# Optimization experiments

Measured on AMD Instinct MI355X. Metric: run time of the kernel, lower is better.

Reference implementation:

```python
import jax, jax.numpy as jnp
import numpy as np

# ---- SS2D hyperparameters (match init_kwargs) ----
B, H, W, D_MODEL = 4, 64, 64, 96
D_STATE = 16
SSM_RATIO = 2
D_INNER = SSM_RATIO * D_MODEL          # 192
DT_RANK = -(-D_MODEL // 16)            # ceil(96/16) = 6
K = 4                                  # 4-way cross scan
D_CONV = 3
LN_EPS = 1e-5


def setup_inputs() -> dict:
    key = jax.random.key(0)
    ks = jax.random.split(key, 8)
    r = lambda i, shape, s: jax.random.normal(ks[i], shape, dtype=jnp.float32) * s
    return {
        "x": jax.random.normal(ks[0], (B, H, W, D_MODEL), dtype=jnp.float32),
        # in_proj: Linear(d_model -> 2*d_inner), bias=False
        "in_proj_w": r(1, (2 * D_INNER, D_MODEL), 0.05),
        # depthwise conv2d: (out=d_inner, in/groups=1, kh, kw), padding 1
        "conv_w": r(2, (D_INNER, 1, D_CONV, D_CONV), 0.1),
        "conv_b": jnp.zeros((D_INNER,), jnp.float32),
        # x_proj_weight: (K, dt_rank + 2*d_state, d_inner)
        "x_proj_weight": r(3, (K, DT_RANK + 2 * D_STATE, D_INNER), 0.05),
        # dt_projs: (K, d_inner, dt_rank) weight, (K, d_inner) bias
        "dt_projs_weight": r(4, (K, D_INNER, DT_RANK), 0.2),
        "dt_projs_bias": r(5, (K, D_INNER), 0.1),
        # A_log = log(arange(1..N)) repeated over K*d_inner channels
        "A_logs": jnp.tile(jnp.log(jnp.arange(1, D_STATE + 1, dtype=jnp.float32))[None, :],
                           (K * D_INNER, 1)),
        "Ds": jnp.ones((K * D_INNER,), jnp.float32),
        "out_norm_w": jnp.ones((D_INNER,), jnp.float32),
        "out_norm_b": jnp.zeros((D_INNER,), jnp.float32),
        # out_proj: Linear(d_inner -> d_model), bias=False
        "out_proj_w": r(6, (D_MODEL, D_INNER), 0.05),
    }


def _cross_scan(x):
    # x: (b, d, h, w) -> xs: (b, 4, d, L)  [row-major, col-major, and their flips]
    b, d, h, w = x.shape
    x0 = x.reshape(b, d, h * w)
    x1 = jnp.swapaxes(x, 2, 3).reshape(b, d, h * w)
    return jnp.stack([x0, x1, x0[..., ::-1], x1[..., ::-1]], axis=1)


def _cross_merge(ys, h, w):
    # ys: (b, 4, d, h, w) -> y: (b, d, L)
    b, k, d = ys.shape[0], ys.shape[1], ys.shape[2]
    ys = ys.reshape(b, k, d, h * w)
    ys = ys[:, 0:2] + ys[:, 2:4][..., ::-1]
    y1 = jnp.swapaxes(ys[:, 1].reshape(b, d, w, h), 2, 3).reshape(b, d, h * w)
    return ys[:, 0] + y1


def _selective_scan(u, dts, A, Bs, Cs, Dskip, delta_bias):
    # u, dts: (b, K, d, L); A: (K, d, N); Bs, Cs: (b, K, N, L)
    # Dskip, delta_bias: (K, d)
    delta = jax.nn.softplus(dts + delta_bias[None, :, :, None])
    u_l = jnp.moveaxis(u, -1, 0)        # (L, b, K, d)
    delta_l = jnp.moveaxis(delta, -1, 0)
    B_l = jnp.moveaxis(Bs, -1, 0)       # (L, b, K, N)
    C_l = jnp.moveaxis(Cs, -1, 0)

    def step(hst, inputs):
        ul, dl, bl, cl = inputs
        dA = jnp.exp(dl[..., None] * A)                       # (b,K,d,N)
        hst = hst * dA + (dl * ul)[..., None] * bl[:, :, None, :]
        y = jnp.einsum('bkdn,bkn->bkd', hst, cl)
        return hst, y

    h0 = jnp.zeros(u_l.shape[1:] + (A.shape[-1],), u.dtype)
    _, ys = jax.lax.scan(step, h0, (u_l, delta_l, B_l, C_l))  # ys: (L,b,K,d)
    ys = jnp.moveaxis(ys, 0, -1)                              # (b,K,d,L)
    return ys + Dskip[None, :, :, None] * u


def reference(x, in_proj_w, conv_w, conv_b, x_proj_weight, dt_projs_weight,
              dt_projs_bias, A_logs, Ds, out_norm_w, out_norm_b, out_proj_w):
    b, h, w, _ = x.shape
    # in_proj then split into ssm branch and gate z
    xz = x @ in_proj_w.T                          # (b,h,w,2*d_inner)
    xin, z = jnp.split(xz, 2, axis=-1)
    # depthwise conv2d (NCHW, OIHW, groups=d_inner) + SiLU
    xc = jnp.transpose(xin, (0, 3, 1, 2))         # (b,d,h,w)
    xc = jax.lax.conv_general_dilated(xc, conv_w, (1, 1), 'SAME',
                                      feature_group_count=D_INNER)
    xc = jax.nn.silu(xc + conv_b[None, :, None, None])

    # cross_selective_scan
    xs = _cross_scan(xc)                                          # (b,4,d,L)
    x_dbl = jnp.einsum('bkdl,kcd->bkcl', xs, x_proj_weight)
    dts, Bs, Cs = jnp.split(x_dbl, [DT_RANK, DT_RANK + D_STATE], axis=2)
    dts = jnp.einsum('bkrl,kdr->bkdl', dts, dt_projs_weight)
    A = -jnp.exp(A_logs).reshape(K, D_INNER, D_STATE)
    ys = _selective_scan(xs, dts, A, Bs, Cs,
                         Ds.reshape(K, D_INNER), dt_projs_bias)   # (b,4,d,L)
    y = _cross_merge(ys.reshape(b, K, D_INNER, h, w), h, w)       # (b,d,L)
    y = jnp.transpose(y, (0, 2, 1)).reshape(b, h, w, D_INNER)

    # out_norm (LayerNorm over d_inner)
    mu = y.mean(-1, keepdims=True)
    var = y.var(-1, keepdims=True)
    y = (y - mu) * jax.lax.rsqrt(var + LN_EPS) * out_norm_w + out_norm_b

    # gate + out_proj
    y = y * jax.nn.silu(z)
    return y @ out_proj_w.T                        # (b,h,w,d_model)
```

## Files before the change

### kernel.cpp

```cpp
#include <hip/hip_runtime.h>
#include <hip/hip_bf16.h>

#define DEV static __device__ __forceinline__

DEV float silu(float x){ return x / (1.f + __expf(-x)); }

typedef __attribute__((ext_vector_type(8))) short bf16x8;
typedef __attribute__((ext_vector_type(4))) float f32x4;

DEV unsigned short f2bf(float f){
    unsigned u = __float_as_uint(f);
    u += 0x7FFF + ((u >> 16) & 1);
    return (unsigned short)(u >> 16);
}
DEV float bf(const unsigned short* p){ return __uint_as_float(((unsigned)(*p)) << 16); }

#define BB 4
#define LL 4096
#define DM 96
#define DI 192
#define NS 16
#define KK 4
#define RR 6
#define C38 38
#define NC 64
#define CL 64
#define NCOMB 224

#define OFF_XIN   0
#define OFF_Z     (OFF_XIN + BB*LL*DI)
#define OFF_XC    (OFF_Z + BB*LL*DI)
#define OFF_DELTA (OFF_XC + BB*LL*DI)
#define OFF_BC    (OFF_DELTA + BB*KK*LL*DI)
#define OFF_YS    (OFF_BC + BB*KK*LL*32)
#define OFF_S     (OFF_YS + BB*KK*LL*DI)
#define OFF_WB    (OFF_S + BB*KK*NC*DI)
#define OFF_CWT   (OFF_WB + 18432)
#define OFF_WC    (OFF_CWT + 1728)
#define OFF_WO    (OFF_WC + 86016)
#define OFF_HLOC  OFF_XIN

DEV int pos_of(int k, int t){
    int pr = ((t & 63) << 6) | (t >> 6);
    int p  = (k & 1) ? pr : t;
    if (k & 2) p = LL - 1 - p;
    return p;
}

__global__ __launch_bounds__(256) void k_prep(const float* __restrict__ win, const float* __restrict__ cw,
                                              const float* __restrict__ xpw, const float* __restrict__ dtw,
                                              const float* __restrict__ wout,
                                              unsigned short* __restrict__ winb, float* __restrict__ cwT,
                                              unsigned short* __restrict__ wcomb, unsigned short* __restrict__ woutb){
    int i = blockIdx.x * 256 + threadIdx.x;
    if (i < 384*DM) winb[i] = f2bf(win[i]);
    if (i < 9*DI){ int tap = i / DI, d = i - tap*DI; cwT[i] = cw[d*9 + tap]; }
    if (i < DM*DI) woutb[i] = f2bf(wout[i]);
    if (i < KK*NCOMB*DI){
        int kk = i % DI; int j = (i / DI) % NCOMB; int k = i / (DI*NCOMB);
        float v;
        if (j < DI){
            v = 0.f;
            const float* dtwp = dtw + ((long)k*DI + j)*RR;
            const float* xp   = xpw + (long)k*C38*DI + kk;
#pragma unroll
            for (int r = 0; r < RR; ++r) v += dtwp[r] * xp[(long)r*DI];
        } else {
            v = xpw[(long)k*C38*DI + (long)(6 + j - DI)*DI + kk];
        }
        wcomb[i] = f2bf(v);
    }
}

__global__ __launch_bounds__(256) void k_inproj(const float* __restrict__ x, const unsigned short* __restrict__ winb,
                                                float* __restrict__ xin, float* __restrict__ z){
    __shared__ unsigned short xsb[16*104];
    int tid = threadIdx.x;
    int r0 = blockIdx.x * 16;
    const float* xrow = x + (long)r0 * DM;
    for (int i = tid; i < 16*DM; i += 256){
        int r = i / DM, d = i - r*DM;
        xsb[r*104 + d] = f2bf(xrow[i]);
    }
    __syncthreads();
    int wv = tid >> 6, l = tid & 63;
    int lrow = l & 15, kg = l >> 4;
    int nc0 = wv * 96;
    f32x4 acc[6];
#pragma unroll
    for (int j = 0; j < 6; ++j) acc[j] = (f32x4){0,0,0,0};
    const unsigned short* arow = &xsb[lrow*104 + kg*8];
#pragma unroll
    for (int kk = 0; kk < 3; ++kk){
        bf16x8 af = *(const bf16x8*)(arow + kk*32);
#pragma unroll
        for (int j = 0; j < 6; ++j){
            int col = nc0 + j*16 + lrow;
            bf16x8 bfr = *(const bf16x8*)(winb + (long)col*DM + kg*8 + kk*32);
            acc[j] = __builtin_amdgcn_mfma_f32_16x16x32_bf16(af, bfr, acc[j], 0,0,0);
        }
    }
#pragma unroll
    for (int j = 0; j < 6; ++j){
        int col = nc0 + j*16 + lrow;
#pragma unroll
        for (int reg = 0; reg < 4; ++reg){
            int row = r0 + kg*4 + reg;
            float v = acc[j][reg];
            if (col < DI) xin[(long)row*DI + col] = v;
            else          z[(long)row*DI + (col - DI)] = v;
        }
    }
}

__global__ __launch_bounds__(256) void k_conv(const float* __restrict__ xin, const float* __restrict__ cwT,
                                              const float* __restrict__ cb, float* __restrict__ xc){
    int g = blockIdx.x * 256 + threadIdx.x;
    int dq = g % 48; int d0 = dq * 4;
    int l = (g / 48) % LL;
    int b = g / (48 * LL);
    int h = l >> 6, wwi = l & 63;
    float4 acc = *(const float4*)(cb + d0);
    const float* base = xin + (long)b * LL * DI + d0;
#pragma unroll
    for (int dy = 0; dy < 3; ++dy){
        int hh = h + dy - 1;
        if (hh < 0 || hh >= 64) continue;
#pragma unroll
        for (int dx = 0; dx < 3; ++dx){
            int wx = wwi + dx - 1;
            if (wx < 0 || wx >= 64) continue;
            float4 xv = *(const float4*)(base + (long)(hh*64 + wx)*DI);
            float4 wv = *(const float4*)(cwT + (dy*3 + dx)*DI + d0);
            acc.x += xv.x*wv.x; acc.y += xv.y*wv.y; acc.z += xv.z*wv.z; acc.w += xv.w*wv.w;
        }
    }
    float4 o;
    o.x = silu(acc.x); o.y = silu(acc.y); o.z = silu(acc.z); o.w = silu(acc.w);
    *(float4*)(xc + ((long)b*LL + l)*DI + d0) = o;
}

#define XP 200
__global__ __launch_bounds__(256) void k_xdbl(const float* __restrict__ xc, const unsigned short* __restrict__ wcomb,
                                              const float* __restrict__ dtb,
                                              unsigned short* __restrict__ delta, float* __restrict__ bc2){
    __shared__ unsigned short xsb[64*XP];
    int tid = threadIdx.x;
    int bk   = blockIdx.x >> 6;
    int tile = blockIdx.x & 63;
    int b = bk >> 2, k = bk & 3;
    int t0 = tile * 64;
    for (int i = tid; i < 64*48; i += 256){
        int r = i / 48, q = i - r*48;
        int p = pos_of(k, t0 + r);
        float4 v = *(const float4*)(xc + ((long)b*LL + p)*DI + q*4);
        ushort4 o;
        o.x = f2bf(v.x); o.y = f2bf(v.y); o.z = f2bf(v.z); o.w = f2bf(v.w);
        *(ushort4*)(&xsb[r*XP + q*4]) = o;
    }
    __syncthreads();

    int wv = tid >> 6, l = tid & 63;
    int lrow = l & 15, kgrp = l >> 4;
    int ch = wv & 1, rh = wv >> 1;
    f32x4 acc[2][7];
#pragma unroll
    for (int rt = 0; rt < 2; ++rt)
#pragma unroll
        for (int j = 0; j < 7; ++j) acc[rt][j] = (f32x4){0,0,0,0};
    const unsigned short* arow0 = &xsb[(rh*32 + lrow)*XP + kgrp*8];
    const unsigned short* arow1 = &xsb[(rh*32 + 16 + lrow)*XP + kgrp*8];
    const unsigned short* wb = wcomb + (long)k*NCOMB*DI + ((long)ch*112 + lrow)*DI + kgrp*8;
#pragma unroll
    for (int ks = 0; ks < 6; ++ks){
        bf16x8 bfr[7];
#pragma unroll
        for (int nt = 0; nt < 7; ++nt)
            bfr[nt] = *(const bf16x8*)(wb + (long)nt*16*DI + ks*32);
        bf16x8 a0 = *(const bf16x8*)(arow0 + ks*32);
        bf16x8 a1 = *(const bf16x8*)(arow1 + ks*32);
#pragma unroll
        for (int nt = 0; nt < 7; ++nt)
            acc[0][nt] = __builtin_amdgcn_mfma_f32_16x16x32_bf16(a0, bfr[nt], acc[0][nt], 0,0,0);
#pragma unroll
        for (int nt = 0; nt < 7; ++nt)
            acc[1][nt] = __builtin_amdgcn_mfma_f32_16x16x32_bf16(a1, bfr[nt], acc[1][nt], 0,0,0);
    }
#pragma unroll
    for (int rt = 0; rt < 2; ++rt){
        long obase = (long)bk*LL + t0 + rh*32 + rt*16 + kgrp*4;
#pragma unroll
        for (int nt = 0; nt < 7; ++nt){
            int col = ch*112 + nt*16 + lrow;
            if (col < DI){
                float bias = dtb[k*DI + col];
#pragma unroll
                for (int reg = 0; reg < 4; ++reg){
                    float raw = acc[rt][nt][reg] + bias;
                    float sp = (raw > 15.f) ? raw : __logf(1.f + __expf(raw));
                    delta[(obase + reg)*DI + col] = f2bf(sp);
                }
            } else {
                int q = col - DI;
#pragma unroll
                for (int reg = 0; reg < 4; ++reg)
                    bc2[(obase + reg)*32 + q] = acc[rt][nt][reg];
            }
        }
    }
}

__global__ __launch_bounds__(192) void k_scanA(const unsigned short* __restrict__ delta, const float* __restrict__ bc2,
                                               const float* __restrict__ xc, const float* __restrict__ alog,
                                               float* __restrict__ hloc, float* __restrict__ Ssum){
    int d = threadIdx.x;
    int bid = blockIdx.x;
    int c = bid & 63; int bk = bid >> 6;
    int b = bk >> 2, k = bk & 3;
    float a[NS]; bool fast = true;
#pragma unroll
    for (int n = 0; n < NS; ++n){
        a[n] = -__expf(alog[(k*DI + d)*NS + n]);
        fast = fast && (fabsf(a[n] + (float)(n + 1)) < 1e-4f*(float)(n + 1));
    }
    int t0 = c * CL;
    int p0, st;
    if (k == 0){ p0 = t0;         st = 1;   }
    else if (k == 1){ p0 = c;     st = 64;  }
    else if (k == 2){ p0 = LL-1-t0; st = -1;  }
    else            { p0 = LL-1-c;  st = -64; }
    const unsigned short* dep = delta + ((long)bk*LL + t0)*DI + d;
    const float* bcp = bc2   + ((long)bk*LL + t0)*32;
    const float* up  = xc + ((long)b*LL + p0)*DI + d;
    long ustep = (long)st * DI;
    float h[NS];
#pragma unroll
    for (int n = 0; n < NS; ++n) h[n] = 0.f;
    float S = 0.f;
    if (fast){
        float de = bf(dep), u = *up;
        const float4* bq = (const float4*)bcp;
        float4 b0 = bq[0], b1 = bq[1], b2 = bq[2], b3 = bq[3];
        for (int i = 0; i < CL; ++i){
            dep += DI; up += ustep; bcp += 32;
            float de_n = bf(dep);
            float u_n  = *up;
            const float4* bqn = (const float4*)bcp;
            float4 b0n = bqn[0], b1n = bqn[1], b2n = bqn[2], b3n = bqn[3];
            float P[NS];
            P[0] = __expf(-de);
            P[1] = P[0]*P[0];
#pragma unroll
            for (int n = 2; n < NS; ++n) P[n] = P[(n-1)>>1] * P[n-1-((n-1)>>1)];
            float du = de * u;
            S += de;
            float bb[NS] = {b0.x,b0.y,b0.z,b0.w, b1.x,b1.y,b1.z,b1.w,
                            b2.x,b2.y,b2.z,b2.w, b3.x,b3.y,b3.z,b3.w};
#pragma unroll
            for (int n = 0; n < NS; ++n) h[n] = h[n]*P[n] + du*bb[n];
            de = de_n; u = u_n; b0 = b0n; b1 = b1n; b2 = b2n; b3 = b3n;
        }
    } else {
        for (int i = 0; i < CL; ++i){
            float de = bf(dep);
            float u  = *up;
            const float4* bq = (const float4*)bcp;
            float4 b0 = bq[0], b1 = bq[1], b2 = bq[2], b3 = bq[3];
            float du = de * u;
            S += de;
            float bb[NS] = {b0.x,b0.y,b0.z,b0.w, b1.x,b1.y,b1.z,b1.w,
                            b2.x,b2.y,b2.z,b2.w, b3.x,b3.y,b3.z,b3.w};
#pragma unroll
            for (int n = 0; n < NS; ++n){ float dA = __expf(de*a[n]); h[n] = h[n]*dA + du*bb[n]; }
            dep += DI; up += ustep; bcp += 32;
        }
    }
    long ho = (((long)bk*NC + c)*DI + d)*NS;
#pragma unroll
    for (int q = 0; q < 4; ++q)
        *(float4*)(hloc + ho + q*4) = make_float4(h[q*4],h[q*4+1],h[q*4+2],h[q*4+3]);
    Ssum[((long)bk*NC + c)*DI + d] = S;
}

__global__ __launch_bounds__(256) void k_scanB(float* __restrict__ hloc, const float* __restrict__ Ssum,
                                               const float* __restrict__ alog){
    int gid = blockIdx.x * 256 + threadIdx.x;
    int dn = gid % (DI*NS);
    int bk = gid / (DI*NS);
    int d = dn >> 4, n = dn & 15;
    int k = bk & 3;
    float a = -__expf(alog[(k*DI + d)*NS + n]);
    float h = 0.f;
    long o     = (long)bk * NC * DI * NS + dn;
    long sbase = (long)bk * NC * DI + d;
    float Sc  = Ssum[sbase];
    float tmp = hloc[o];
    for (int c = 0; c < NC; ++c){
        long o_n = o + (long)DI*NS;
        float Sc_n  = Ssum[sbase + (long)(c+1)*DI];
        float tmp_n = hloc[o_n];
        float P = __expf(a * Sc);
        hloc[o] = h;
        h = h * P + tmp;
        o = o_n; Sc = Sc_n; tmp = tmp_n;
    }
}

__global__ __launch_bounds__(192) void k_scanC(const unsigned short* __restrict__ delta, const float* __restrict__ bc2,
                                               const float* __restrict__ xc, const float* __restrict__ alog,
                                               const float* __restrict__ hloc, unsigned short* __restrict__ ys){
    int d = threadIdx.x;
    int bid = blockIdx.x;
    int c = bid & 63; int bk = bid >> 6;
    int b = bk >> 2, k = bk & 3;
    float a[NS]; bool fast = true;
#pragma unroll
    for (int n = 0; n < NS; ++n){
        a[n] = -__expf(alog[(k*DI + d)*NS + n]);
        fast = fast && (fabsf(a[n] + (float)(n + 1)) < 1e-4f*(float)(n + 1));
    }
    int t0 = c * CL;
    int p0, st;
    if (k == 0){ p0 = t0;         st = 1;   }
    else if (k == 1){ p0 = c;     st = 64;  }
    else if (k == 2){ p0 = LL-1-t0; st = -1;  }
    else            { p0 = LL-1-c;  st = -64; }
    const unsigned short* dep = delta + ((long)bk*LL + t0)*DI + d;
    const float* bcp = bc2   + ((long)bk*LL + t0)*32;
    const float* up  = xc + ((long)b*LL + p0)*DI + d;
    unsigned short* yp = ys + ((long)bk*LL + p0)*DI + d;
    long ustep = (long)st * DI;
    long ho = (((long)bk*NC + c)*DI + d)*NS;
    float h[NS];
#pragma unroll
    for (int q = 0; q < 4; ++q){
        float4 hv = *(const float4*)(hloc + ho + q*4);
        h[q*4] = hv.x; h[q*4+1] = hv.y; h[q*4+2] = hv.z; h[q*4+3] = hv.w;
    }
    if (fast){
        float de = bf(dep), u = *up;
        const float4* bq = (const float4*)bcp;
        float4 b0 = bq[0], b1 = bq[1], b2 = bq[2], b3 = bq[3];
        float4 c0 = bq[4], c1 = bq[5], c2 = bq[6], c3 = bq[7];
        for (int i = 0; i < CL; ++i){
            dep += DI; up += ustep; bcp += 32;
            float de_n = bf(dep);
            float u_n  = *up;
            const float4* bqn = (const float4*)bcp;
            float4 b0n = bqn[0], b1n = bqn[1], b2n = bqn[2], b3n = bqn[3];
            float4 c0n = bqn[4], c1n = bqn[5], c2n = bqn[6], c3n = bqn[7];
            float P[NS];
            P[0] = __expf(-de);
            P[1] = P[0]*P[0];
#pragma unroll
            for (int n = 2; n < NS; ++n) P[n] = P[(n-1)>>1] * P[n-1-((n-1)>>1)];
            float du = de * u;
            float bb[NS] = {b0.x,b0.y,b0.z,b0.w, b1.x,b1.y,b1.z,b1.w,
                            b2.x,b2.y,b2.z,b2.w, b3.x,b3.y,b3.z,b3.w};
            float cc[NS] = {c0.x,c0.y,c0.z,c0.w, c1.x,c1.y,c1.z,c1.w,
                            c2.x,c2.y,c2.z,c2.w, c3.x,c3.y,c3.z,c3.w};
            float y = 0.f;
#pragma unroll
            for (int n = 0; n < NS; ++n){ h[n] = h[n]*P[n] + du*bb[n]; y += h[n]*cc[n]; }
            *yp = f2bf(y);
            yp += ustep;
            de = de_n; u = u_n;
            b0 = b0n; b1 = b1n; b2 = b2n; b3 = b3n;
            c0 = c0n; c1 = c1n; c2 = c2n; c3 = c3n;
        }
    } else {
        for (int i = 0; i < CL; ++i){
            float de = bf(dep);
            float u  = *up;
            const float4* bq = (const float4*)bcp;
            float4 b0 = bq[0], b1 = bq[1], b2 = bq[2], b3 = bq[3];
            float4 c0 = bq[4], c1 = bq[5], c2 = bq[6], c3 = bq[7];
            float du = de * u;
            float bb[NS] = {b0.x,b0.y,b0.z,b0.w, b1.x,b1.y,b1.z,b1.w,
                            b2.x,b2.y,b2.z,b2.w, b3.x,b3.y,b3.z,b3.w};
            float cc[NS] = {c0.x,c0.y,c0.z,c0.w, c1.x,c1.y,c1.z,c1.w,
                            c2.x,c2.y,c2.z,c2.w, c3.x,c3.y,c3.z,c3.w};
            float y = 0.f;
#pragma unroll
            for (int n = 0; n < NS; ++n){ float dA = __expf(de*a[n]); h[n] = h[n]*dA + du*bb[n]; y += h[n]*cc[n]; }
            *yp = f2bf(y);
            dep += DI; up += ustep; yp += ustep; bcp += 32;
        }
    }
}

__global__ __launch_bounds__(256) void k_fuse(const unsigned short* __restrict__ ys, const float* __restrict__ xc,
                                              const float* __restrict__ z, const float* __restrict__ Dsk,
                                              const float* __restrict__ lnw, const float* __restrict__ lnb,
                                              const unsigned short* __restrict__ woutb, float* __restrict__ out){
    __shared__ unsigned short gt[32*200];
    int tid = threadIdx.x;
    int wv = tid >> 6, l = tid & 63;
    int b  = blockIdx.x / (LL/32);
    int p0 = (blockIdx.x % (LL/32)) * 32;
    float sumD[3], lw[3], lb[3];
#pragma unroll
    for (int q = 0; q < 3; ++q){
        int d = l + q*64;
        sumD[q] = Dsk[d] + Dsk[DI + d] + Dsk[2*DI + d] + Dsk[3*DI + d];
        lw[q] = lnw[d]; lb[q] = lnb[d];
    }
    for (int pass = 0; pass < 8; ++pass){
        int pl = wv*8 + pass;
        int p = p0 + pl;
        long base = (long)b*LL + p;
        float yv[3], zv[3];
        float s = 0.f, sq = 0.f;
#pragma unroll
        for (int q = 0; q < 3; ++q){
            int d = l + q*64;
            long yo = ((long)(b*4)*LL + p)*DI + d;
            float y = bf(ys + yo) + bf(ys + yo + (long)LL*DI)
                    + bf(ys + yo + 2L*LL*DI) + bf(ys + yo + 3L*LL*DI);
            y += xc[base*DI + d] * sumD[q];
            zv[q] = z[base*DI + d];
            yv[q] = y; s += y; sq += y*y;
        }
#pragma unroll
        for (int m = 32; m > 0; m >>= 1){ s += __shfl_xor(s, m, 64); sq += __shfl_xor(sq, m, 64); }
        float mu = s / DI, var = sq / DI - mu*mu;
        float rs = rsqrtf(var + 1e-5f);
#pragma unroll
        for (int q = 0; q < 3; ++q){
            int d = l + q*64;
            float yn = (yv[q] - mu)*rs*lw[q] + lb[q];
            gt[pl*200 + d] = f2bf(yn * silu(zv[q]));
        }
    }
    __syncthreads();
    int lrow = l & 15, kg = l >> 4;
    int rt = wv & 1, cp = wv >> 1;
    f32x4 acc[3];
#pragma unroll
    for (int j = 0; j < 3; ++j) acc[j] = (f32x4){0,0,0,0};
    const unsigned short* arow = &gt[(rt*16 + lrow)*200 + kg*8];
    const unsigned short* wbase = woutb + ((long)cp*48 + lrow)*DI + kg*8;
#pragma unroll
    for (int ks = 0; ks < 6; ++ks){
        bf16x8 af = *(const bf16x8*)(arow + ks*32);
#pragma unroll
        for (int nt = 0; nt < 3; ++nt){
            bf16x8 bfr = *(const bf16x8*)(wbase + (long)nt*16*DI + ks*32);
            acc[nt] = __builtin_amdgcn_mfma_f32_16x16x32_bf16(af, bfr, acc[nt], 0,0,0);
        }
    }
#pragma unroll
    for (int nt = 0; nt < 3; ++nt){
        int m = cp*48 + nt*16 + lrow;
#pragma unroll
        for (int reg = 0; reg < 4; ++reg){
            int pl = rt*16 + kg*4 + reg;
            out[((long)b*LL + p0 + pl)*DM + m] = acc[nt][reg];
        }
    }
}

extern "C" void kernel_launch(void* const* d_in, const int* in_sizes, int n_in,
                              void* d_out, int out_size, void* d_ws, size_t ws_size,
                              hipStream_t stream){
    (void)in_sizes; (void)n_in; (void)out_size; (void)ws_size;
    const float* x    = (const float*)d_in[0];
    const float* win  = (const float*)d_in[1];
    const float* cw   = (const float*)d_in[2];
    const float* cb   = (const float*)d_in[3];
    const float* xpw  = (const float*)d_in[4];
    const float* dtw  = (const float*)d_in[5];
    const float* dtb  = (const float*)d_in[6];
    const float* alog = (const float*)d_in[7];
    const float* ds   = (const float*)d_in[8];
    const float* lnw  = (const float*)d_in[9];
    const float* lnb  = (const float*)d_in[10];
    const float* wout = (const float*)d_in[11];

    float* ws    = (float*)d_ws;
    float* xin   = ws + OFF_XIN;
    float* z     = ws + OFF_Z;
    float* xc    = ws + OFF_XC;
    unsigned short* delta = (unsigned short*)(ws + OFF_DELTA);
    float* bc2   = ws + OFF_BC;
    unsigned short* ysb = (unsigned short*)(ws + OFF_YS);
    float* Ssum  = ws + OFF_S;
    unsigned short* winb  = (unsigned short*)(ws + OFF_WB);
    float* cwT   = ws + OFF_CWT;
    unsigned short* wcomb = (unsigned short*)(ws + OFF_WC);
    unsigned short* woutb = (unsigned short*)(ws + OFF_WO);
    float* hloc  = ws + OFF_HLOC;

    k_prep  <<<dim3(672),  dim3(256), 0, stream>>>(win, cw, xpw, dtw, wout, winb, cwT, wcomb, woutb);
    k_inproj<<<dim3(1024), dim3(256), 0, stream>>>(x, winb, xin, z);
    k_conv  <<<dim3(3072), dim3(256), 0, stream>>>(xin, cwT, cb, xc);
    k_xdbl  <<<dim3(1024), dim3(256), 0, stream>>>(xc, wcomb, dtb, delta, bc2);
    k_scanA <<<dim3(1024), dim3(192), 0, stream>>>(delta, bc2, xc, alog, hloc, Ssum);
    k_scanB <<<dim3(192),  dim3(256), 0, stream>>>(hloc, Ssum, alog);
    k_scanC <<<dim3(1024), dim3(192), 0, stream>>>(delta, bc2, xc, alog, hloc, ysb);
    k_fuse  <<<dim3(512),  dim3(256), 0, stream>>>(ysb, xc, z, ds, lnw, lnb, woutb,
                                                   (float*)d_out);
}
```

Baseline: 163.0 us.

## Fuse x_proj/dt_proj GEMM into both scan passes, recomputing through LDS

Removes the standalone k_xdbl kernel and the global delta/B/C buffers. Each scan pass (A and C) now recomputes the per-chunk MFMA projection into shared memory and runs the chunk recurrence from LDS. This cuts the large global write and re-read of delta and B/C. In exchange the GEMM runs twice, each block holds about 56KB of LDS, which limits occupancy, and only 192 of 256 threads run the scan. The scan input u is also now read as bf16 instead of fp32.

```diff
diff --git a/kernel.cpp b/kernel.cpp
--- a/kernel.cpp
+++ b/kernel.cpp
@@ -30,9 +30,7 @@
 #define OFF_XIN   0
 #define OFF_Z     (OFF_XIN + BB*LL*DI)
 #define OFF_XC    (OFF_Z + BB*LL*DI)
-#define OFF_DELTA (OFF_XC + BB*LL*DI)
-#define OFF_BC    (OFF_DELTA + BB*KK*LL*DI)
-#define OFF_YS    (OFF_BC + BB*KK*LL*32)
+#define OFF_YS    (OFF_XC + BB*LL*DI)
 #define OFF_S     (OFF_YS + BB*KK*LL*DI)
 #define OFF_WB    (OFF_S + BB*KK*NC*DI)
 #define OFF_CWT   (OFF_WB + 18432)
@@ -141,15 +139,74 @@
 }
 
 #define XP 200
-__global__ __launch_bounds__(256) void k_xdbl(const float* __restrict__ xc, const unsigned short* __restrict__ wcomb,
-                                              const float* __restrict__ dtb,
-                                              unsigned short* __restrict__ delta, float* __restrict__ bc2){
+
+template<int BS, bool WANT_C>
+DEV void gemm_phase(int tid, int k, const unsigned short* __restrict__ wcomb,
+                    const float* __restrict__ dtb,
+                    const unsigned short* xsb, unsigned short* dlds, float* blds){
+    int wv = tid >> 6, l = tid & 63;
+    int lrow = l & 15, kgrp = l >> 4;
+    int ch = wv & 1, rh = wv >> 1;
+    f32x4 acc[2][7];
+#pragma unroll
+    for (int rt = 0; rt < 2; ++rt)
+#pragma unroll
+        for (int j = 0; j < 7; ++j) acc[rt][j] = (f32x4){0,0,0,0};
+    const unsigned short* arow0 = &xsb[(rh*32 + lrow)*XP + kgrp*8];
+    const unsigned short* arow1 = &xsb[(rh*32 + 16 + lrow)*XP + kgrp*8];
+    const unsigned short* wb = wcomb + (long)k*NCOMB*DI + ((long)ch*112 + lrow)*DI + kgrp*8;
+#pragma unroll
+    for (int ks = 0; ks < 6; ++ks){
+        bf16x8 bfr[7];
+#pragma unroll
+        for (int nt = 0; nt < 7; ++nt)
+            bfr[nt] = *(const bf16x8*)(wb + (long)nt*16*DI + ks*32);
+        bf16x8 a0 = *(const bf16x8*)(arow0 + ks*32);
+        bf16x8 a1 = *(const bf16x8*)(arow1 + ks*32);
+#pragma unroll
+        for (int nt = 0; nt < 7; ++nt)
+            acc[0][nt] = __builtin_amdgcn_mfma_f32_16x16x32_bf16(a0, bfr[nt], acc[0][nt], 0,0,0);
+#pragma unroll
+        for (int nt = 0; nt < 7; ++nt)
+            acc[1][nt] = __builtin_amdgcn_mfma_f32_16x16x32_bf16(a1, bfr[nt], acc[1][nt], 0,0,0);
+    }
+#pragma unroll
+    for (int rt = 0; rt < 2; ++rt){
+        int rowb = rh*32 + rt*16 + kgrp*4;
+#pragma unroll
+        for (int nt = 0; nt < 7; ++nt){
+            int col = ch*112 + nt*16 + lrow;
+            if (col < DI){
+                float bias = dtb[k*DI + col];
+#pragma unroll
+                for (int reg = 0; reg < 4; ++reg){
+                    float raw = acc[rt][nt][reg] + bias;
+                    float sp = (raw > 15.f) ? raw : __logf(1.f + __expf(raw));
+                    dlds[(rowb + reg)*XP + col] = f2bf(sp);
+                }
+            } else {
+                int q = col - DI;
+                if (WANT_C || q < 16){
+#pragma unroll
+                    for (int reg = 0; reg < 4; ++reg)
+                        blds[(rowb + reg)*BS + q] = acc[rt][nt][reg];
+                }
+            }
+        }
+    }
+}
+
+#define BSA 20
+__global__ __launch_bounds__(256) void k_scanAf(const float* __restrict__ xc, const unsigned short* __restrict__ wcomb,
+                                                const float* __restrict__ dtb, const float* __restrict__ alog,
+                                                float* __restrict__ hloc, float* __restrict__ Ssum){
     __shared__ unsigned short xsb[64*XP];
+    __shared__ unsigned short dlds[64*XP];
+    __shared__ float blds[64*BSA];
     int tid = threadIdx.x;
-    int bk   = blockIdx.x >> 6;
-    int tile = blockIdx.x & 63;
+    int c = blockIdx.x & 63; int bk = blockIdx.x >> 6;
     int b = bk >> 2, k = bk & 3;
-    int t0 = tile * 64;
+    int t0 = c * CL;
     for (int i = tid; i < 64*48; i += 256){
         int r = i / 48, q = i - r*48;
         int p = pos_of(k, t0 + r);
@@ -159,127 +216,58 @@
         *(ushort4*)(&xsb[r*XP + q*4]) = o;
     }
     __syncthreads();
-
-    int wv = tid >> 6, l = tid & 63;
-    int lrow = l & 15, kgrp = l >> 4;
-    int ch = wv & 1, rh = wv >> 1;
-    f32x4 acc[2][7];
-#pragma unroll
-    for (int rt = 0; rt < 2; ++rt)
-#pragma unroll
-        for (int j = 0; j < 7; ++j) acc[rt][j] = (f32x4){0,0,0,0};
-    const unsigned short* arow0 = &xsb[(rh*32 + lrow)*XP + kgrp*8];
-    const unsigned short* arow1 = &xsb[(rh*32 + 16 + lrow)*XP + kgrp*8];
-    const unsigned short* wb = wcomb + (long)k*NCOMB*DI + ((long)ch*112 + lrow)*DI + kgrp*8;
-#pragma unroll
-    for (int ks = 0; ks < 6; ++ks){
-        bf16x8 bfr[7];
-#pragma unroll
-        for (int nt = 0; nt < 7; ++nt)
-            bfr[nt] = *(const bf16x8*)(wb + (long)nt*16*DI + ks*32);
-        bf16x8 a0 = *(const bf16x8*)(arow0 + ks*32);
-        bf16x8 a1 = *(const bf16x8*)(arow1 + ks*32);
-#pragma unroll
-        for (int nt = 0; nt < 7; ++nt)
-            acc[0][nt] = __builtin_amdgcn_mfma_f32_16x16x32_bf16(a0, bfr[nt], acc[0][nt], 0,0,0);
-#pragma unroll
-        for (int nt = 0; nt < 7; ++nt)
-            acc[1][nt] = __builtin_amdgcn_mfma_f32_16x16x32_bf16(a1, bfr[nt], acc[1][nt], 0,0,0);
-    }
-#pragma unroll
-    for (int rt = 0; rt < 2; ++rt){
-        long obase = (long)bk*LL + t0 + rh*32 + rt*16 + kgrp*4;
-#pragma unroll
-        for (int nt = 0; nt < 7; ++nt){
-            int col = ch*112 + nt*16 + lrow;
-            if (col < DI){
-                float bias = dtb[k*DI + col];
-#pragma unroll
-                for (int reg = 0; reg < 4; ++reg){
-                    float raw = acc[rt][nt][reg] + bias;
-                    float sp = (raw > 15.f) ? raw : __logf(1.f + __expf(raw));
-                    delta[(obase + reg)*DI + col] = f2bf(sp);
-                }
-            } else {
-                int q = col - DI;
-#pragma unroll
-                for (int reg = 0; reg < 4; ++reg)
-                    bc2[(obase + reg)*32 + q] = acc[rt][nt][reg];
+    gemm_phase<BSA, false>(tid, k, wcomb, dtb, xsb, dlds, blds);
+    __syncthreads();
+    if (tid < DI){
+        int d = tid;
+        float a[NS]; bool fast = true;
+#pragma unroll
+        for (int n = 0; n < NS; ++n){
+            a[n] = -__expf(alog[(k*DI + d)*NS + n]);
+            fast = fast && (fabsf(a[n] + (float)(n + 1)) < 1e-4f*(float)(n + 1));
+        }
+        float h[NS];
+#pragma unroll
+        for (int n = 0; n < NS; ++n) h[n] = 0.f;
+        float S = 0.f;
+        if (fast){
+            for (int i = 0; i < CL; ++i){
+                float de = bf(&dlds[i*XP + d]);
+                float u  = bf(&xsb[i*XP + d]);
+                const float4* bq = (const float4*)&blds[i*BSA];
+                float4 b0 = bq[0], b1 = bq[1], b2 = bq[2], b3 = bq[3];
+                float P[NS];
+                P[0] = __expf(-de);
+                P[1] = P[0]*P[0];
+#pragma unroll
+                for (int n = 2; n < NS; ++n) P[n] = P[(n-1)>>1] * P[n-1-((n-1)>>1)];
+                float du = de * u;
+                S += de;
+                float bb[NS] = {b0.x,b0.y,b0.z,b0.w, b1.x,b1.y,b1.z,b1.w,
+                                b2.x,b2.y,b2.z,b2.w, b3.x,b3.y,b3.z,b3.w};
+#pragma unroll
+                for (int n = 0; n < NS; ++n) h[n] = h[n]*P[n] + du*bb[n];
             }
-        }
-    }
-}
-
-__global__ __launch_bounds__(192) void k_scanA(const unsigned short* __restrict__ delta, const float* __restrict__ bc2,
-                                               const float* __restrict__ xc, const float* __restrict__ alog,
-                                               float* __restrict__ hloc, float* __restrict__ Ssum){
-    int d = threadIdx.x;
-    int bid = blockIdx.x;
-    int c = bid & 63; int bk = bid >> 6;
-    int b = bk >> 2, k = bk & 3;
-    float a[NS]; bool fast = true;
-#pragma unroll
-    for (int n = 0; n < NS; ++n){
-        a[n] = -__expf(alog[(k*DI + d)*NS + n]);
-        fast = fast && (fabsf(a[n] + (float)(n + 1)) < 1e-4f*(float)(n + 1));
-    }
-    int t0 = c * CL;
-    int p0, st;
-    if (k == 0){ p0 = t0;         st = 1;   }
-    else if (k == 1){ p0 = c;     st = 64;  }
-    else if (k == 2){ p0 = LL-1-t0; st = -1;  }
-    else            { p0 = LL-1-c;  st = -64; }
-    const unsigned short* dep = delta + ((long)bk*LL + t0)*DI + d;
-    const float* bcp = bc2   + ((long)bk*LL + t0)*32;
-    const float* up  = xc + ((long)b*LL + p0)*DI + d;
-    long ustep = (long)st * DI;
-    float h[NS];
-#pragma unroll
-    for (int n = 0; n < NS; ++n) h[n] = 0.f;
-    float S = 0.f;
-    if (fast){
-        float de = bf(dep), u = *up;
-        const float4* bq = (const float4*)bcp;
-        float4 b0 = bq[0], b1 = bq[1], b2 = bq[2], b3 = bq[3];
-        for (int i = 0; i < CL; ++i){
-            dep += DI; up += ustep; bcp += 32;
-            float de_n = bf(dep);
-            float u_n  = *up;
-            const float4* bqn = (const float4*)bcp;
-            float4 b0n = bqn[0], b1n = bqn[1], b2n = bqn[2], b3n = bqn[3];
-            float P[NS];
-            P[0] = __expf(-de);
-            P[1] = P[0]*P[0];
-#pragma unroll
-            for (int n = 2; n < NS; ++n) P[n] = P[(n-1)>>1] * P[n-1-((n-1)>>1)];
-            float du = de * u;
-            S += de;
-            float bb[NS] = {b0.x,b0.y,b0.z,b0.w, b1.x,b1.y,b1.z,b1.w,
-                            b2.x,b2.y,b2.z,b2.w, b3.x,b3.y,b3.z,b3.w};
-#pragma unroll
-            for (int n = 0; n < NS; ++n) h[n] = h[n]*P[n] + du*bb[n];
-            de = de_n; u = u_n; b0 = b0n; b1 = b1n; b2 = b2n; b3 = b3n;
-        }
-    } else {
-        for (int i = 0; i < CL; ++i){
-            float de = bf(dep);
-            float u  = *up;
-            const float4* bq = (const float4*)bcp;
-            float4 b0 = bq[0], b1 = bq[1], b2 = bq[2], b3 = bq[3];
-            float du = de * u;
-            S += de;
-            float bb[NS] = {b0.x,b0.y,b0.z,b0.w, b1.x,b1.y,b1.z,b1.w,
-                            b2.x,b2.y,b2.z,b2.w, b3.x,b3.y,b3.z,b3.w};
-#pragma unroll
-            for (int n = 0; n < NS; ++n){ float dA = __expf(de*a[n]); h[n] = h[n]*dA + du*bb[n]; }
-            dep += DI; up += ustep; bcp += 32;
-        }
-    }
-    long ho = (((long)bk*NC + c)*DI + d)*NS;
-#pragma unroll
-    for (int q = 0; q < 4; ++q)
-        *(float4*)(hloc + ho + q*4) = make_float4(h[q*4],h[q*4+1],h[q*4+2],h[q*4+3]);
-    Ssum[((long)bk*NC + c)*DI + d] = S;
+        } else {
+            for (int i = 0; i < CL; ++i){
+                float de = bf(&dlds[i*XP + d]);
+                float u  = bf(&xsb[i*XP + d]);
+                const float4* bq = (const float4*)&blds[i*BSA];
+                float4 b0 = bq[0], b1 = bq[1], b2 = bq[2], b3 = bq[3];
+                float du = de * u;
+                S += de;
+                float bb[NS] = {b0.x,b0.y,b0.z,b0.w, b1.x,b1.y,b1.z,b1.w,
+                                b2.x,b2.y,b2.z,b2.w, b3.x,b3.y,b3.z,b3.w};
+#pragma unroll
+                for (int n = 0; n < NS; ++n){ float dA = __expf(de*a[n]); h[n] = h[n]*dA + du*bb[n]; }
+            }
+        }
+        long ho = (((long)bk*NC + c)*DI + d)*NS;
+#pragma unroll
+        for (int q = 0; q < 4; ++q)
+            *(float4*)(hloc + ho + q*4) = make_float4(h[q*4],h[q*4+1],h[q*4+2],h[q*4+3]);
+        Ssum[((long)bk*NC + c)*DI + d] = S;
+    }
 }
 
 __global__ __launch_bounds__(256) void k_scanB(float* __restrict__ hloc, const float* __restrict__ Ssum,
@@ -306,85 +294,91 @@
     }
 }
 
-__global__ __launch_bounds__(192) void k_scanC(const unsigned short* __restrict__ delta, const float* __restrict__ bc2,
-                                               const float* __restrict__ xc, const float* __restrict__ alog,
-                                               const float* __restrict__ hloc, unsigned short* __restrict__ ys){
-    int d = threadIdx.x;
-    int bid = blockIdx.x;
-    int c = bid & 63; int bk = bid >> 6;
+#define BSC 36
+__global__ __launch_bounds__(256) void k_scanCf(const float* __restrict__ xc, const unsigned short* __restrict__ wcomb,
+                                                const float* __restrict__ dtb, const float* __restrict__ alog,
+                                                const float* __restrict__ hloc, unsigned short* __restrict__ ys){
+    __shared__ unsigned short xsb[64*XP];
+    __shared__ unsigned short dlds[64*XP];
+    __shared__ float blds[64*BSC];
+    int tid = threadIdx.x;
+    int c = blockIdx.x & 63; int bk = blockIdx.x >> 6;
     int b = bk >> 2, k = bk & 3;
-    float a[NS]; bool fast = true;
-#pragma unroll
-    for (int n = 0; n < NS; ++n){
-        a[n] = -__expf(alog[(k*DI + d)*NS + n]);
-        fast = fast && (fabsf(a[n] + (float)(n + 1)) < 1e-4f*(float)(n + 1));
-    }
     int t0 = c * CL;
-    int p0, st;
-    if (k == 0){ p0 = t0;         st = 1;   }
-    else if (k == 1){ p0 = c;     st = 64;  }
-    else if (k == 2){ p0 = LL-1-t0; st = -1;  }
-    else            { p0 = LL-1-c;  st = -64; }
-    const unsigned short* dep = delta + ((long)bk*LL + t0)*DI + d;
-    const float* bcp = bc2   + ((long)bk*LL + t0)*32;
-    const float* up  = xc + ((long)b*LL + p0)*DI + d;
-    unsigned short* yp = ys + ((long)bk*LL + p0)*DI + d;
-    long ustep = (long)st * DI;
-    long ho = (((long)bk*NC + c)*DI + d)*NS;
-    float h[NS];
-#pragma unroll
-    for (int q = 0; q < 4; ++q){
-        float4 hv = *(const float4*)(hloc + ho + q*4);
-        h[q*4] = hv.x; h[q*4+1] = hv.y; h[q*4+2] = hv.z; h[q*4+3] = hv.w;
-    }
-    if (fast){
-        float de = bf(dep), u = *up;
-        const float4* bq = (const float4*)bcp;
-        float4 b0 = bq[0], b1 = bq[1], b2 = bq[2], b3 = bq[3];
-        float4 c0 = bq[4], c1 = bq[5], c2 = bq[6], c3 = bq[7];
-        for (int i = 0; i < CL; ++i){
-            dep += DI; up += ustep; bcp += 32;
-            float de_n = bf(dep);
-            float u_n  = *up;
-            const float4* bqn = (const float4*)bcp;
-            float4 b0n = bqn[0], b1n = bqn[1], b2n = bqn[2], b3n = bqn[3];
-            float4 c0n = bqn[4], c1n = bqn[5], c2n = bqn[6], c3n = bqn[7];
-            float P[NS];
-            P[0] = __expf(-de);
-            P[1] = P[0]*P[0];
-#pragma unroll
-            for (int n = 2; n < NS; ++n) P[n] = P[(n-1)>>1] * P[n-1-((n-1)>>1)];
-            float du = de * u;
-            float bb[NS] = {b0.x,b0.y,b0.z,b0.w, b1.x,b1.y,b1.z,b1.w,
-                            b2.x,b2.y,b2.z,b2.w, b3.x,b3.y,b3.z,b3.w};
-            float cc[NS] = {c0.x,c0.y,c0.z,c0.w, c1.x,c1.y,c1.z,c1.w,
-                            c2.x,c2.y,c2.z,c2.w, c3.x,c3.y,c3.z,c3.w};
-            float y = 0.f;
-#pragma unroll
-            for (int n = 0; n < NS; ++n){ h[n] = h[n]*P[n] + du*bb[n]; y += h[n]*cc[n]; }
-            *yp = f2bf(y);
-            yp += ustep;
-            de = de_n; u = u_n;
-            b0 = b0n; b1 = b1n; b2 = b2n; b3 = b3n;
-            c0 = c0n; c1 = c1n; c2 = c2n; c3 = c3n;
-        }
-    } else {
-        for (int i = 0; i < CL; ++i){
-            float de = bf(dep);
-            float u  = *up;
-            const float4* bq = (const float4*)bcp;
-            float4 b0 = bq[0], b1 = bq[1], b2 = bq[2], b3 = bq[3];
-            float4 c0 = bq[4], c1 = bq[5], c2 = bq[6], c3 = bq[7];
-            float du = de * u;
-            float bb[NS] = {b0.x,b0.y,b0.z,b0.w, b1.x,b1.y,b1.z,b1.w,
-                            b2.x,b2.y,b2.z,b2.w, b3.x,b3.y,b3.z,b3.w};
-            float cc[NS] = {c0.x,c0.y,c0.z,c0.w, c1.x,c1.y,c1.z,c1.w,
-                            c2.x,c2.y,c2.z,c2.w, c3.x,c3.y,c3.z,c3.w};
-            float y = 0.f;
-#pragma unroll
-            for (int n = 0; n < NS; ++n){ float dA = __expf(de*a[n]); h[n] = h[n]*dA + du*bb[n]; y += h[n]*cc[n]; }
-            *yp = f2bf(y);
-            dep += DI; up += ustep; yp += ustep; bcp += 32;
+    for (int i = tid; i < 64*48; i += 256){
+        int r = i / 48, q = i - r*48;
+        int p = pos_of(k, t0 + r);
+        float4 v = *(const float4*)(xc + ((long)b*LL + p)*DI + q*4);
+        ushort4 o;
+        o.x = f2bf(v.x); o.y = f2bf(v.y); o.z = f2bf(v.z); o.w = f2bf(v.w);
+        *(ushort4*)(&xsb[r*XP + q*4]) = o;
+    }
+    __syncthreads();
+    gemm_phase<BSC, true>(tid, k, wcomb, dtb, xsb, dlds, blds);
+    __syncthreads();
+    if (tid < DI){
+        int d = tid;
+        float a[NS]; bool fast = true;
+#pragma unroll
+        for (int n = 0; n < NS; ++n){
+            a[n] = -__expf(alog[(k*DI + d)*NS + n]);
+            fast = fast && (fabsf(a[n] + (float)(n + 1)) < 1e-4f*(float)(n + 1));
+        }
+        int p0, st;
+        if (k == 0){ p0 = t0;         st = 1;   }
+        else if (k == 1){ p0 = c;     st = 64;  }
+        else if (k == 2){ p0 = LL-1-t0; st = -1;  }
+        else            { p0 = LL-1-c;  st = -64; }
+        unsigned short* yp = ys + ((long)bk*LL + p0)*DI + d;
+        long ustep = (long)st * DI;
+        long ho = (((long)bk*NC + c)*DI + d)*NS;
+        float h[NS];
+#pragma unroll
+        for (int q = 0; q < 4; ++q){
+            float4 hv = *(const float4*)(hloc + ho + q*4);
+            h[q*4] = hv.x; h[q*4+1] = hv.y; h[q*4+2] = hv.z; h[q*4+3] = hv.w;
+        }
+        if (fast){
+            for (int i = 0; i < CL; ++i){
+                float de = bf(&dlds[i*XP + d]);
+                float u  = bf(&xsb[i*XP + d]);
+                const float4* bq = (const float4*)&blds[i*BSC];
+                float4 b0 = bq[0], b1 = bq[1], b2 = bq[2], b3 = bq[3];
+                float4 c0 = bq[4], c1 = bq[5], c2 = bq[6], c3 = bq[7];
+                float P[NS];
+                P[0] = __expf(-de);
+                P[1] = P[0]*P[0];
+#pragma unroll
+                for (int n = 2; n < NS; ++n) P[n] = P[(n-1)>>1] * P[n-1-((n-1)>>1)];
+                float du = de * u;
+                float bb[NS] = {b0.x,b0.y,b0.z,b0.w, b1.x,b1.y,b1.z,b1.w,
+                                b2.x,b2.y,b2.z,b2.w, b3.x,b3.y,b3.z,b3.w};
+                float cc[NS] = {c0.x,c0.y,c0.z,c0.w, c1.x,c1.y,c1.z,c1.w,
+                                c2.x,c2.y,c2.z,c2.w, c3.x,c3.y,c3.z,c3.w};
+                float y = 0.f;
+#pragma unroll
+                for (int n = 0; n < NS; ++n){ h[n] = h[n]*P[n] + du*bb[n]; y += h[n]*cc[n]; }
+                *yp = f2bf(y);
+                yp += ustep;
+            }
+        } else {
+            for (int i = 0; i < CL; ++i){
+                float de = bf(&dlds[i*XP + d]);
+                float u  = bf(&xsb[i*XP + d]);
+                const float4* bq = (const float4*)&blds[i*BSC];
+                float4 b0 = bq[0], b1 = bq[1], b2 = bq[2], b3 = bq[3];
+                float4 c0 = bq[4], c1 = bq[5], c2 = bq[6], c3 = bq[7];
+                float du = de * u;
+                float bb[NS] = {b0.x,b0.y,b0.z,b0.w, b1.x,b1.y,b1.z,b1.w,
+                                b2.x,b2.y,b2.z,b2.w, b3.x,b3.y,b3.z,b3.w};
+                float cc[NS] = {c0.x,c0.y,c0.z,c0.w, c1.x,c1.y,c1.z,c1.w,
+                                c2.x,c2.y,c2.z,c2.w, c3.x,c3.y,c3.z,c3.w};
+                float y = 0.f;
+#pragma unroll
+                for (int n = 0; n < NS; ++n){ float dA = __expf(de*a[n]); h[n] = h[n]*dA + du*bb[n]; y += h[n]*cc[n]; }
+                *yp = f2bf(y);
+                yp += ustep;
+            }
         }
     }
 }
@@ -481,8 +475,6 @@
     float* xin   = ws + OFF_XIN;
     float* z     = ws + OFF_Z;
     float* xc    = ws + OFF_XC;
-    unsigned short* delta = (unsigned short*)(ws + OFF_DELTA);
-    float* bc2   = ws + OFF_BC;
     unsigned short* ysb = (unsigned short*)(ws + OFF_YS);
     float* Ssum  = ws + OFF_S;
     unsigned short* winb  = (unsigned short*)(ws + OFF_WB);
@@ -494,10 +486,9 @@
     k_prep  <<<dim3(672),  dim3(256), 0, stream>>>(win, cw, xpw, dtw, wout, winb, cwT, wcomb, woutb);
     k_inproj<<<dim3(1024), dim3(256), 0, stream>>>(x, winb, xin, z);
     k_conv  <<<dim3(3072), dim3(256), 0, stream>>>(xin, cwT, cb, xc);
-    k_xdbl  <<<dim3(1024), dim3(256), 0, stream>>>(xc, wcomb, dtb, delta, bc2);
-    k_scanA <<<dim3(1024), dim3(192), 0, stream>>>(delta, bc2, xc, alog, hloc, Ssum);
+    k_scanAf<<<dim3(1024), dim3(256), 0, stream>>>(xc, wcomb, dtb, alog, hloc, Ssum);
     k_scanB <<<dim3(192),  dim3(256), 0, stream>>>(hloc, Ssum, alog);
-    k_scanC <<<dim3(1024), dim3(192), 0, stream>>>(delta, bc2, xc, alog, hloc, ysb);
+    k_scanCf<<<dim3(1024), dim3(256), 0, stream>>>(xc, wcomb, dtb, alog, hloc, ysb);
     k_fuse  <<<dim3(512),  dim3(256), 0, stream>>>(ysb, xc, z, ds, lnw, lnb, woutb,
                                                    (float*)d_out);
 }
```

After: 179.2 us. 1.1x slower.

## Store delta/BC in spatial order and share xc tile across all four scan directions

Applied to the files above, without the earlier changes.

k_xdbl now loads one spatial tile of xc per block and computes the projections for all four scan directions from it, with 8 waves (4 directions × 2 column halves). Delta and B/C are written in spatial position order rather than per-direction scan order. The scan kernels therefore stride through delta/bc with the same direction-dependent step as xc. This cuts the xc gather work fourfold and removes the permuted loads, but the scans for the column-major directions now read delta/bc with large strides, and each k_xdbl thread holds more accumulators, which can lower occupancy.

```diff
diff --git a/kernel.cpp b/kernel.cpp
--- a/kernel.cpp
+++ b/kernel.cpp
@@ -39,13 +39,6 @@
 #define OFF_WC    (OFF_CWT + 1728)
 #define OFF_WO    (OFF_WC + 86016)
 #define OFF_HLOC  OFF_XIN
-
-DEV int pos_of(int k, int t){
-    int pr = ((t & 63) << 6) | (t >> 6);
-    int p  = (k & 1) ? pr : t;
-    if (k & 2) p = LL - 1 - p;
-    return p;
-}
 
 __global__ __launch_bounds__(256) void k_prep(const float* __restrict__ win, const float* __restrict__ cw,
                                               const float* __restrict__ xpw, const float* __restrict__ dtw,
@@ -141,19 +134,17 @@
 }
 
 #define XP 200
-__global__ __launch_bounds__(256) void k_xdbl(const float* __restrict__ xc, const unsigned short* __restrict__ wcomb,
+__global__ __launch_bounds__(512) void k_xdbl(const float* __restrict__ xc, const unsigned short* __restrict__ wcomb,
                                               const float* __restrict__ dtb,
                                               unsigned short* __restrict__ delta, float* __restrict__ bc2){
     __shared__ unsigned short xsb[64*XP];
     int tid = threadIdx.x;
-    int bk   = blockIdx.x >> 6;
+    int b    = blockIdx.x >> 6;
     int tile = blockIdx.x & 63;
-    int b = bk >> 2, k = bk & 3;
-    int t0 = tile * 64;
-    for (int i = tid; i < 64*48; i += 256){
+    int p0 = tile * 64;
+    for (int i = tid; i < 64*48; i += 512){
         int r = i / 48, q = i - r*48;
-        int p = pos_of(k, t0 + r);
-        float4 v = *(const float4*)(xc + ((long)b*LL + p)*DI + q*4);
+        float4 v = *(const float4*)(xc + ((long)b*LL + p0 + r)*DI + q*4);
         ushort4 o;
         o.x = f2bf(v.x); o.y = f2bf(v.y); o.z = f2bf(v.z); o.w = f2bf(v.w);
         *(ushort4*)(&xsb[r*XP + q*4]) = o;
@@ -161,15 +152,13 @@
     __syncthreads();
 
     int wv = tid >> 6, l = tid & 63;
+    int k = wv & 3, ch = wv >> 2;
     int lrow = l & 15, kgrp = l >> 4;
-    int ch = wv & 1, rh = wv >> 1;
-    f32x4 acc[2][7];
-#pragma unroll
-    for (int rt = 0; rt < 2; ++rt)
+    f32x4 acc[4][7];
+#pragma unroll
+    for (int rt = 0; rt < 4; ++rt)
 #pragma unroll
         for (int j = 0; j < 7; ++j) acc[rt][j] = (f32x4){0,0,0,0};
-    const unsigned short* arow0 = &xsb[(rh*32 + lrow)*XP + kgrp*8];
-    const unsigned short* arow1 = &xsb[(rh*32 + 16 + lrow)*XP + kgrp*8];
     const unsigned short* wb = wcomb + (long)k*NCOMB*DI + ((long)ch*112 + lrow)*DI + kgrp*8;
 #pragma unroll
     for (int ks = 0; ks < 6; ++ks){
@@ -177,18 +166,20 @@
 #pragma unroll
         for (int nt = 0; nt < 7; ++nt)
             bfr[nt] = *(const bf16x8*)(wb + (long)nt*16*DI + ks*32);
-        bf16x8 a0 = *(const bf16x8*)(arow0 + ks*32);
-        bf16x8 a1 = *(const bf16x8*)(arow1 + ks*32);
-#pragma unroll
-        for (int nt = 0; nt < 7; ++nt)
-            acc[0][nt] = __builtin_amdgcn_mfma_f32_16x16x32_bf16(a0, bfr[nt], acc[0][nt], 0,0,0);
-#pragma unroll
-        for (int nt = 0; nt < 7; ++nt)
-            acc[1][nt] = __builtin_amdgcn_mfma_f32_16x16x32_bf16(a1, bfr[nt], acc[1][nt], 0,0,0);
-    }
-#pragma unroll
-    for (int rt = 0; rt < 2; ++rt){
-        long obase = (long)bk*LL + t0 + rh*32 + rt*16 + kgrp*4;
+        bf16x8 a[4];
+#pragma unroll
+        for (int rt = 0; rt < 4; ++rt)
+            a[rt] = *(const bf16x8*)(&xsb[(rt*16 + lrow)*XP + kgrp*8 + ks*32]);
+#pragma unroll
+        for (int rt = 0; rt < 4; ++rt)
+#pragma unroll
+            for (int nt = 0; nt < 7; ++nt)
+                acc[rt][nt] = __builtin_amdgcn_mfma_f32_16x16x32_bf16(a[rt], bfr[nt], acc[rt][nt], 0,0,0);
+    }
+    int bk = b*4 + k;
+#pragma unroll
+    for (int rt = 0; rt < 4; ++rt){
+        long obase = (long)bk*LL + p0 + rt*16 + kgrp*4;
 #pragma unroll
         for (int nt = 0; nt < 7; ++nt){
             int col = ch*112 + nt*16 + lrow;
@@ -229,10 +220,11 @@
     else if (k == 1){ p0 = c;     st = 64;  }
     else if (k == 2){ p0 = LL-1-t0; st = -1;  }
     else            { p0 = LL-1-c;  st = -64; }
-    const unsigned short* dep = delta + ((long)bk*LL + t0)*DI + d;
-    const float* bcp = bc2   + ((long)bk*LL + t0)*32;
+    const unsigned short* dep = delta + ((long)bk*LL + p0)*DI + d;
+    const float* bcp = bc2   + ((long)bk*LL + p0)*32;
     const float* up  = xc + ((long)b*LL + p0)*DI + d;
     long ustep = (long)st * DI;
+    long bstep = (long)st * 32;
     float h[NS];
 #pragma unroll
     for (int n = 0; n < NS; ++n) h[n] = 0.f;
@@ -242,7 +234,7 @@
         const float4* bq = (const float4*)bcp;
         float4 b0 = bq[0], b1 = bq[1], b2 = bq[2], b3 = bq[3];
         for (int i = 0; i < CL; ++i){
-            dep += DI; up += ustep; bcp += 32;
+            dep += ustep; up += ustep; bcp += bstep;
             float de_n = bf(dep);
             float u_n  = *up;
             const float4* bqn = (const float4*)bcp;
@@ -272,7 +264,7 @@
                             b2.x,b2.y,b2.z,b2.w, b3.x,b3.y,b3.z,b3.w};
 #pragma unroll
             for (int n = 0; n < NS; ++n){ float dA = __expf(de*a[n]); h[n] = h[n]*dA + du*bb[n]; }
-            dep += DI; up += ustep; bcp += 32;
+            dep += ustep; up += ustep; bcp += bstep;
         }
     }
     long ho = (((long)bk*NC + c)*DI + d)*NS;
@@ -325,11 +317,12 @@
     else if (k == 1){ p0 = c;     st = 64;  }
     else if (k == 2){ p0 = LL-1-t0; st = -1;  }
     else            { p0 = LL-1-c;  st = -64; }
-    const unsigned short* dep = delta + ((long)bk*LL + t0)*DI + d;
-    const float* bcp = bc2   + ((long)bk*LL + t0)*32;
+    const unsigned short* dep = delta + ((long)bk*LL + p0)*DI + d;
+    const float* bcp = bc2   + ((long)bk*LL + p0)*32;
     const float* up  = xc + ((long)b*LL + p0)*DI + d;
     unsigned short* yp = ys + ((long)bk*LL + p0)*DI + d;
     long ustep = (long)st * DI;
+    long bstep = (long)st * 32;
     long ho = (((long)bk*NC + c)*DI + d)*NS;
     float h[NS];
 #pragma unroll
@@ -343,7 +336,7 @@
         float4 b0 = bq[0], b1 = bq[1], b2 = bq[2], b3 = bq[3];
         float4 c0 = bq[4], c1 = bq[5], c2 = bq[6], c3 = bq[7];
         for (int i = 0; i < CL; ++i){
-            dep += DI; up += ustep; bcp += 32;
+            dep += ustep; up += ustep; bcp += bstep;
             float de_n = bf(dep);
             float u_n  = *up;
             const float4* bqn = (const float4*)bcp;
@@ -384,7 +377,7 @@
 #pragma unroll
             for (int n = 0; n < NS; ++n){ float dA = __expf(de*a[n]); h[n] = h[n]*dA + du*bb[n]; y += h[n]*cc[n]; }
             *yp = f2bf(y);
-            dep += DI; up += ustep; yp += ustep; bcp += 32;
+            dep += ustep; up += ustep; yp += ustep; bcp += bstep;
         }
     }
 }
@@ -494,7 +487,7 @@
     k_prep  <<<dim3(672),  dim3(256), 0, stream>>>(win, cw, xpw, dtw, wout, winb, cwT, wcomb, woutb);
     k_inproj<<<dim3(1024), dim3(256), 0, stream>>>(x, winb, xin, z);
     k_conv  <<<dim3(3072), dim3(256), 0, stream>>>(xin, cwT, cb, xc);
-    k_xdbl  <<<dim3(1024), dim3(256), 0, stream>>>(xc, wcomb, dtb, delta, bc2);
+    k_xdbl  <<<dim3(256),  dim3(512), 0, stream>>>(xc, wcomb, dtb, delta, bc2);
     k_scanA <<<dim3(1024), dim3(192), 0, stream>>>(delta, bc2, xc, alog, hloc, Ssum);
     k_scanB <<<dim3(192),  dim3(256), 0, stream>>>(hloc, Ssum, alog);
     k_scanC <<<dim3(1024), dim3(192), 0, stream>>>(delta, bc2, xc, alog, hloc, ysb);
```

New measurement: 146.9 us. 1.11x faster.
